# Kernel optimization log

Hardware: AMD Instinct MI355X
Metric: run time of the kernel (lower is better)

Reference implementation:

```python
import jax, jax.numpy as jnp
import numpy as np

N = 8192  # source points
M = 8192  # target points
T = 8     # RL path steps


def setup_inputs() -> dict:
    key = jax.random.key(0)
    ks = jax.random.split(key, 6)
    return {
        "source": jax.random.normal(ks[0], (N, 3), jnp.float32),
        "target": jax.random.normal(ks[1], (M, 3), jnp.float32),
        "label": jax.random.uniform(ks[2], (N,), jnp.float32),
        "trans_m": 0.01 * jax.random.normal(ks[3], (T, N, 3), jnp.float32),
        "path_m": jax.random.uniform(ks[4], (T, N), jnp.float32),
        "path_maxprob_m": jax.random.uniform(ks[5], (T, N), jnp.float32, minval=0.05, maxval=1.0),
    }


def _catculate_loss2(p1, p2):
    # p1: [N,3], p2: [M,3] -> pairwise squared distances [N,M]
    dist = jnp.sum((p1[:, None, :] - p2[None, :, :]) ** 2, axis=-1)
    dist_min = jnp.min(dist, axis=-1)
    dist_max = jnp.max(dist, axis=-1)
    return 0.99 * dist_min + 0.01 * dist_max  # [N]


def reference(source, target, label, trans_m, path_m, path_maxprob_m):
    p = 0.002
    L0 = 0.4
    lammda = 0.05
    gamma = 0.99
    Tn = path_m.shape[0]

    trans_end = trans_m[-1]
    points_denoise = source - trans_end
    loss_start = _catculate_loss2(source, target)
    loss_end = _catculate_loss2(points_denoise, target)
    loss_dt = loss_end - loss_start

    d = jnp.minimum(loss_end / L0, 1.0)  # where(d>1, 1, d)
    l = jnp.exp(-label)

    reward_end = -p * path_m[-1] - (d + lammda * l) * loss_dt  # [N]
    # rewards: [N, T] = per-step path penalties then final reward
    rewards = jnp.concatenate([(-p * path_m[:-1]).T, reward_end[:, None]], axis=-1)

    logp = jnp.log(path_maxprob_m)  # [T, N]

    # discounted return scan, iterating i = T-1 .. 0
    def step(carry, xs):
        R, L = carry
        lp, r = xs
        R = gamma * R + lp * (r + 0.02)
        return (R, L - R), None

    init = (jnp.zeros_like(reward_end), jnp.zeros_like(reward_end))
    (_, L), _ = jax.lax.scan(step, init, (logp[::-1], rewards.T[::-1]))
    loss = L / Tn  # [N]
    return jnp.mean(loss)
```

## Files before the change

kernel.cpp:

```cpp
#include <hip/hip_runtime.h>
#include <math.h>

#define TPB 256
#define TILE 256

__global__ __launch_bounds__(TPB) void k1_partial_minmax(
    const float* __restrict__ source,
    const float* __restrict__ target,
    const float* __restrict__ trans_m,
    float* __restrict__ part,
    int N, int M, int T, int S)
{
    const int chunk = M / S;
    const int i = blockIdx.x * TPB + threadIdx.x;
    const int s = blockIdx.y;

    __shared__ float tgt[TILE * 3];

    const float sx = source[i * 3 + 0];
    const float sy = source[i * 3 + 1];
    const float sz = source[i * 3 + 2];
    const long teoff = (long)(T - 1) * N * 3 + (long)i * 3;
    const float ex = sx - trans_m[teoff + 0];
    const float ey = sy - trans_m[teoff + 1];
    const float ez = sz - trans_m[teoff + 2];

    float mins = 3.402823e38f, maxs = -3.402823e38f;
    float mine = 3.402823e38f, maxe = -3.402823e38f;

    const int t_begin = s * chunk;
    const int t_end   = t_begin + chunk;

    for (int t0 = t_begin; t0 < t_end; t0 += TILE) {
        __syncthreads();
        for (int k = threadIdx.x; k < TILE * 3; k += TPB)
            tgt[k] = target[(long)t0 * 3 + k];
        __syncthreads();

        #pragma unroll 4
        for (int j = 0; j < TILE; ++j) {
            const float tx = tgt[j * 3 + 0];
            const float ty = tgt[j * 3 + 1];
            const float tz = tgt[j * 3 + 2];
            float dx = sx - tx, dy = sy - ty, dz = sz - tz;
            float ds = dx * dx + dy * dy + dz * dz;
            mins = fminf(mins, ds);
            maxs = fmaxf(maxs, ds);
            dx = ex - tx; dy = ey - ty; dz = ez - tz;
            float de = dx * dx + dy * dy + dz * dz;
            mine = fminf(mine, de);
            maxe = fmaxf(maxe, de);
        }
    }

    part[(0 * S + s) * (long)N + i] = mins;
    part[(1 * S + s) * (long)N + i] = maxs;
    part[(2 * S + s) * (long)N + i] = mine;
    part[(3 * S + s) * (long)N + i] = maxe;
}

__global__ __launch_bounds__(TPB) void k2_loss(
    const float* __restrict__ part,
    const float* __restrict__ label,
    const float* __restrict__ path_m,
    const float* __restrict__ path_maxprob_m,
    float* __restrict__ blocksums,
    int N, int S, int T)
{
    const int i = blockIdx.x * TPB + threadIdx.x;

    float mins = 3.402823e38f, maxs = -3.402823e38f;
    float mine = 3.402823e38f, maxe = -3.402823e38f;
    for (int s = 0; s < S; ++s) {
        mins = fminf(mins, part[(0 * S + s) * (long)N + i]);
        maxs = fmaxf(maxs, part[(1 * S + s) * (long)N + i]);
        mine = fminf(mine, part[(2 * S + s) * (long)N + i]);
        maxe = fmaxf(maxe, part[(3 * S + s) * (long)N + i]);
    }

    const float p = 0.002f, L0 = 0.4f, lam = 0.05f, gamma = 0.99f;
    const float loss_start = 0.99f * mins + 0.01f * maxs;
    const float loss_end   = 0.99f * mine + 0.01f * maxe;
    const float loss_dt    = loss_end - loss_start;
    const float d = fminf(loss_end / L0, 1.0f);
    const float l = expf(-label[i]);
    const float reward_end = -p * path_m[(long)(T - 1) * N + i]
                             - (d + lam * l) * loss_dt;

    float R = 0.0f, L = 0.0f;
    for (int t = T - 1; t >= 0; --t) {
        const float r  = (t == T - 1) ? reward_end
                                      : (-p * path_m[(long)t * N + i]);
        const float lp = logf(path_maxprob_m[(long)t * N + i]);
        R = gamma * R + lp * (r + 0.02f);
        L -= R;
    }
    float v = L / (float)T;

    for (int off = 32; off > 0; off >>= 1) v += __shfl_down(v, off, 64);
    __shared__ float red[TPB / 64];
    const int wid = threadIdx.x >> 6, lane = threadIdx.x & 63;
    if (lane == 0) red[wid] = v;
    __syncthreads();
    if (threadIdx.x == 0) {
        float t = 0.0f;
        #pragma unroll
        for (int w = 0; w < TPB / 64; ++w) t += red[w];
        blocksums[blockIdx.x] = t;
    }
}

__global__ void k3_final(const float* __restrict__ blocksums,
                         float* __restrict__ out, int nb, int N)
{
    float v = (threadIdx.x < nb) ? blocksums[threadIdx.x] : 0.0f;
    for (int off = 32; off > 0; off >>= 1) v += __shfl_down(v, off, 64);
    if (threadIdx.x == 0) out[0] = v / (float)N;
}

extern "C" void kernel_launch(void* const* d_in, const int* in_sizes, int n_in,
                              void* d_out, int out_size, void* d_ws, size_t ws_size,
                              hipStream_t stream) {
    const float* source = (const float*)d_in[0];
    const float* target = (const float*)d_in[1];
    const float* label  = (const float*)d_in[2];
    const float* trans  = (const float*)d_in[3];
    const float* path   = (const float*)d_in[4];
    const float* pmax   = (const float*)d_in[5];

    const int N = in_sizes[0] / 3;
    const int M = in_sizes[1] / 3;
    const int T = in_sizes[3] / (N * 3);
    const int nbx = N / TPB;

    int S = 32;
    while (S > 1 && (size_t)(4 * (size_t)S * N + nbx) * sizeof(float) > ws_size)
        S >>= 1;

    float* part      = (float*)d_ws;
    float* blocksums = part + (size_t)4 * S * N;

    k1_partial_minmax<<<dim3(nbx, S), TPB, 0, stream>>>(
        source, target, trans, part, N, M, T, S);
    k2_loss<<<nbx, TPB, 0, stream>>>(
        part, label, path, pmax, blocksums, N, S, T);
    k3_final<<<1, 64, 0, stream>>>(blocksums, (float*)d_out, nbx, N);
}
```

Before: 105.6 us.

## Expand squared distance into norms plus dot product with precomputed target norms

Rewrites each pairwise squared distance as |s|^2 + |t|^2 - 2 s·t. Target norms are precomputed into a float4 shared tile, so the inner loop costs three FMAs per distance instead of subtracts and multiplies, and the source norm is added once after the min/max. It also halves the tile size, raises the target split count to 64 for more blocks, and loads targets as vectorized float4 from LDS. The expansion can cancel catastrophically for nearby points, which changes numerics in the min distance.

```diff
diff --git a/kernel.cpp b/kernel.cpp
--- a/kernel.cpp
+++ b/kernel.cpp
@@ -2,7 +2,7 @@
 #include <math.h>
 
 #define TPB 256
-#define TILE 256
+#define TILE 128
 
 __global__ __launch_bounds__(TPB) void k1_partial_minmax(
     const float* __restrict__ source,
@@ -15,7 +15,7 @@
     const int i = blockIdx.x * TPB + threadIdx.x;
     const int s = blockIdx.y;
 
-    __shared__ float tgt[TILE * 3];
+    __shared__ float4 tgt[TILE];
 
     const float sx = source[i * 3 + 0];
     const float sy = source[i * 3 + 1];
@@ -25,6 +25,11 @@
     const float ey = sy - trans_m[teoff + 1];
     const float ez = sz - trans_m[teoff + 2];
 
+    const float ss = fmaf(sx, sx, fmaf(sy, sy, sz * sz));
+    const float ee = fmaf(ex, ex, fmaf(ey, ey, ez * ez));
+    const float vsx = -2.0f * sx, vsy = -2.0f * sy, vsz = -2.0f * sz;
+    const float vex = -2.0f * ex, vey = -2.0f * ey, vez = -2.0f * ez;
+
     float mins = 3.402823e38f, maxs = -3.402823e38f;
     float mine = 3.402823e38f, maxe = -3.402823e38f;
 
@@ -33,30 +38,35 @@
 
     for (int t0 = t_begin; t0 < t_end; t0 += TILE) {
         __syncthreads();
-        for (int k = threadIdx.x; k < TILE * 3; k += TPB)
-            tgt[k] = target[(long)t0 * 3 + k];
+        for (int j = threadIdx.x; j < TILE; j += TPB) {
+            const float tx = target[(long)(t0 + j) * 3 + 0];
+            const float ty = target[(long)(t0 + j) * 3 + 1];
+            const float tz = target[(long)(t0 + j) * 3 + 2];
+            const float q  = fmaf(tx, tx, fmaf(ty, ty, tz * tz));
+            tgt[j] = make_float4(tx, ty, tz, q);
+        }
         __syncthreads();
 
-        #pragma unroll 4
+        #pragma unroll 8
         for (int j = 0; j < TILE; ++j) {
-            const float tx = tgt[j * 3 + 0];
-            const float ty = tgt[j * 3 + 1];
-            const float tz = tgt[j * 3 + 2];
-            float dx = sx - tx, dy = sy - ty, dz = sz - tz;
-            float ds = dx * dx + dy * dy + dz * dz;
-            mins = fminf(mins, ds);
-            maxs = fmaxf(maxs, ds);
-            dx = ex - tx; dy = ey - ty; dz = ez - tz;
-            float de = dx * dx + dy * dy + dz * dz;
-            mine = fminf(mine, de);
-            maxe = fmaxf(maxe, de);
+            const float4 t = tgt[j];
+            float a = fmaf(vsx, t.x, t.w);
+            a = fmaf(vsy, t.y, a);
+            a = fmaf(vsz, t.z, a);
+            mins = fminf(mins, a);
+            maxs = fmaxf(maxs, a);
+            float b = fmaf(vex, t.x, t.w);
+            b = fmaf(vey, t.y, b);
+            b = fmaf(vez, t.z, b);
+            mine = fminf(mine, b);
+            maxe = fmaxf(maxe, b);
         }
     }
 
-    part[(0 * S + s) * (long)N + i] = mins;
-    part[(1 * S + s) * (long)N + i] = maxs;
-    part[(2 * S + s) * (long)N + i] = mine;
-    part[(3 * S + s) * (long)N + i] = maxe;
+    part[(0 * S + s) * (long)N + i] = mins + ss;
+    part[(1 * S + s) * (long)N + i] = maxs + ss;
+    part[(2 * S + s) * (long)N + i] = mine + ee;
+    part[(3 * S + s) * (long)N + i] = maxe + ee;
 }
 
 __global__ __launch_bounds__(TPB) void k2_loss(
@@ -133,8 +143,9 @@
     const int T = in_sizes[3] / (N * 3);
     const int nbx = N / TPB;
 
-    int S = 32;
-    while (S > 1 && (size_t)(4 * (size_t)S * N + nbx) * sizeof(float) > ws_size)
+    int S = 64;
+    while (S > 1 && ((size_t)(4 * (size_t)S * N + nbx) * sizeof(float) > ws_size
+                     || (M / S) < TILE))
         S >>= 1;
 
     float* part      = (float*)d_ws;
```

New measurement: 105.2 us. No clear change (-0.4%).
